# Optimization experiments

Measured on AMD Instinct MI355X. Metric: run time of the kernel, lower is better.

Reference implementation:

```python
import jax, jax.numpy as jnp
import numpy as np

B, S, N, D = 4, 4, 2048, 2048  # batch, residual streams, seq len, model dim


def rmsnorm(x, gamma, eps=1e-12):
    # F.normalize(x, dim=-1) * sqrt(d) * (gamma + 1)
    n = jnp.sqrt(jnp.sum(x * x, axis=-1, keepdims=True))
    return x / jnp.maximum(n, eps) * (x.shape[-1] ** 0.5) * (gamma + 1.0)


def setup_inputs() -> dict:
    key = jax.random.key(0)
    k0, k1, k2, k3 = jax.random.split(key, 4)
    residuals = jax.random.normal(k0, (B * S, N, D), dtype=jnp.float32)
    gamma = (jax.random.normal(k1, (D,), dtype=jnp.float32) * 0.02)
    # ProjActScale weights are zero-init in the module; use small random values
    # so the dynamic paths are numerically exercised.
    w_alpha = jax.random.normal(k2, (S + 1, D), dtype=jnp.float32) * 0.02
    w_beta = jax.random.normal(k3, (1, D), dtype=jnp.float32) * 0.02
    scale_alpha = jnp.asarray(0.01, dtype=jnp.float32)
    scale_beta = jnp.asarray(0.01, dtype=jnp.float32)
    # static_alpha = cat([init_alpha0, eye(S)], dim=1), layer_index=0 -> one-hot row 0
    init_alpha0 = np.zeros((S, 1), dtype=np.float32)
    init_alpha0[0, 0] = 1.0
    static_alpha = jnp.asarray(np.concatenate([init_alpha0, np.eye(S, dtype=np.float32)], axis=1))
    static_beta = jnp.ones((S,), dtype=jnp.float32)
    return dict(residuals=residuals, gamma=gamma, w_alpha=w_alpha, scale_alpha=scale_alpha,
                static_alpha=static_alpha, w_beta=w_beta, scale_beta=scale_beta,
                static_beta=static_beta)


def reference(residuals, gamma, w_alpha, scale_alpha, static_alpha, w_beta, scale_beta, static_beta):
    bs, n, d = residuals.shape
    s = static_beta.shape[0]
    b = bs // s
    # '(b s) n d -> b n s d'
    x = residuals.reshape(b, s, n, d).transpose(0, 2, 1, 3)
    normed = rmsnorm(x, gamma)
    # dynamic alpha / beta: zero-bias linear -> tanh -> scale
    dyn_alpha = jnp.tanh(jnp.einsum('bnsd,td->bnst', normed, w_alpha)) * scale_alpha
    alpha = dyn_alpha + static_alpha                      # (b, n, s, s+1)
    dyn_beta = jnp.tanh(jnp.einsum('bnsd,od->bnso', normed, w_beta))[..., 0] * scale_beta
    beta = dyn_beta + static_beta                         # (b, n, s)
    # width connection: mix residual streams
    mix = jnp.einsum('bnst,bnsd->bntd', alpha, x)         # (b, n, s+1, d)
    branch_input = mix[:, :, 0, :]                        # (b, n, d)
    res = mix[:, :, 1:, :]                                # (b, n, s, d)
    # identity branch (module has branch=None; the add_residual closure applies this)
    branch_out = branch_input
    # depth connection: outer product with beta, add residuals
    res = branch_out[:, :, None, :] * beta[..., None] + res
    # 'b n s d -> (b s) n d'
    out = res.transpose(0, 2, 1, 3).reshape(bs, n, d)
    return out
```

## Files before the change

### kernel.cpp

```cpp
#include <hip/hip_runtime.h>
#include <math.h>

#define NB 4
#define NS 4
#define NN 2048
#define ND 2048
#define NTHREADS 512
#define KPB 4
#define SQRT_D 45.254833995939045f

typedef float f32x4 __attribute__((ext_vector_type(4)));

#define GLOAD(dst, addr) \
    asm volatile("global_load_dwordx4 %0, %1, off" : "=&v"(dst) : "v"(addr) : "memory")

#define VM_WAIT_PREFETCH() do {                                \
    asm volatile("s_waitcnt vmcnt(4)" ::: "memory");           \
    __builtin_amdgcn_sched_barrier(0); } while (0)

#define SHIP(I, H, M_) {                                      \
    const float keep_ = hi_ ? v[(I)+(H)] : v[(I)];            \
    const float give_ = hi_ ? v[(I)] : v[(I)+(H)];            \
    v[(I)] = keep_ + __shfl_xor(give_, (M_)); }

#define BUTTERFLY()                                                          \
    { const bool hi_ = (lane & 1) != 0;                                      \
      SHIP(0,16,1)  SHIP(1,16,1)  SHIP(2,16,1)  SHIP(3,16,1)                 \
      SHIP(4,16,1)  SHIP(5,16,1)  SHIP(6,16,1)  SHIP(7,16,1)                 \
      SHIP(8,16,1)  SHIP(9,16,1)  SHIP(10,16,1) SHIP(11,16,1)                \
      SHIP(12,16,1) SHIP(13,16,1) SHIP(14,16,1) SHIP(15,16,1) }              \
    { const bool hi_ = (lane & 2) != 0;                                      \
      SHIP(0,8,2) SHIP(1,8,2) SHIP(2,8,2) SHIP(3,8,2)                        \
      SHIP(4,8,2) SHIP(5,8,2) SHIP(6,8,2) SHIP(7,8,2) }                      \
    { const bool hi_ = (lane & 4) != 0;                                      \
      SHIP(0,4,4) SHIP(1,4,4) SHIP(2,4,4) SHIP(3,4,4) }                      \
    { const bool hi_ = (lane & 8) != 0;                                      \
      SHIP(0,2,8) SHIP(1,2,8) }                                              \
    { const bool hi_ = (lane & 16) != 0;                                     \
      SHIP(0,1,16) }

#define ITER(XC0, XC1, XC2, XC3, XN0, XN1, XN2, XN3, K, PREF, WAIT)          \
  {                                                                          \
    if (WAIT) VM_WAIT_PREFETCH();                                            \
    float v[32];                                                             \
    _Pragma("unroll") for (int q = 0; q < 32; ++q) v[q] = 0.f;               \
    {                                                                        \
      f32x4 g4 = *(const f32x4*)(gamma + d);                                 \
      _Pragma("unroll") for (int e = 0; e < 4; ++e) {                        \
        v[0]  = __builtin_fmaf(XC0[e], XC0[e], v[0]);                        \
        v[7]  = __builtin_fmaf(XC1[e], XC1[e], v[7]);                        \
        v[14] = __builtin_fmaf(XC2[e], XC2[e], v[14]);                       \
        v[21] = __builtin_fmaf(XC3[e], XC3[e], v[21]);                       \
      }                                                                      \
      _Pragma("unroll") for (int j = 0; j < 6; ++j) {                        \
        const float* wsrc = (j < 5) ? (w_alpha + (size_t)j * ND + d)         \
                                    : (w_beta + d);                          \
        f32x4 w4 = *(const f32x4*)wsrc;                                      \
        f32x4 wg = w4 + w4 * g4;                        \
        _Pragma("unroll") for (int e = 0; e < 4; ++e) {                      \
          v[1 + j]  = __builtin_fmaf(XC0[e], wg[e], v[1 + j]);               \
          v[8 + j]  = __builtin_fmaf(XC1[e], wg[e], v[8 + j]);               \
          v[15 + j] = __builtin_fmaf(XC2[e], wg[e], v[15 + j]);              \
          v[22 + j] = __builtin_fmaf(XC3[e], wg[e], v[22 + j]);              \
        }                                                                    \
      }                                                                      \
    }                                                                        \
        \
    if (PREF) {                                                              \
      const float* np_ = xp + ((K) + 1) * ND;                                \
      GLOAD(XN0, np_);                                                       \
      GLOAD(XN1, np_ + row_stride);                                          \
      GLOAD(XN2, np_ + 2 * row_stride);                                      \
      GLOAD(XN3, np_ + 3 * row_stride);                                      \
    }                                                                        \
    BUTTERFLY()                                                              \
    const float tot##K = v[0] + __shfl_xor(v[0], 32);                        \
    if (lane < 32) red[wave][bidx] = tot##K;                                 \
    __syncthreads();                                                         \
    if (tid < 24) {                                                          \
      float ssq_ = 0.f, dot_ = 0.f;                                          \
      _Pragma("unroll") for (int w = 0; w < 8; ++w) {                        \
        ssq_ += red[w][es * 7];                                              \
        dot_ += red[w][es * 7 + 1 + ej];                                     \
      }                                                                      \
      const float rs_ = SQRT_D / fmaxf(sqrtf(ssq_), 1e-12f);                 \
      asb[es][ej] = __builtin_fmaf(tanhf(dot_ * rs_),                        \
                                   (ej < 5) ? sa : sb, stat);                \
    }                                                                        \
    __syncthreads();                                                         \
    {                                                                        \
      float M[NS][NS];                                                       \
      _Pragma("unroll") for (int so = 0; so < NS; ++so)                      \
        _Pragma("unroll") for (int si = 0; si < NS; ++si)                    \
          M[so][si] = __builtin_fmaf(asb[so][5], asb[si][0],                 \
                                     asb[si][so + 1]);                       \
      float* op_ = op + (K) * ND;                                            \
      _Pragma("unroll") for (int so = 0; so < NS; ++so) {                    \
        f32x4 o;                                                             \
        _Pragma("unroll") for (int e = 0; e < 4; ++e)                        \
          o[e] = M[so][0] * XC0[e] + M[so][1] * XC1[e]                       \
               + M[so][2] * XC2[e] + M[so][3] * XC3[e];                      \
        __builtin_nontemporal_store(o, (f32x4*)(op_ + (size_t)so * row_stride)); \
      }                                                                      \
    }                                                                        \
  }

__global__ __launch_bounds__(NTHREADS, 4)
void hyperconn_kernel(const float* __restrict__ residuals,
                      const float* __restrict__ gamma,
                      const float* __restrict__ w_alpha,
                      const float* __restrict__ scale_alpha,
                      const float* __restrict__ static_alpha,
                      const float* __restrict__ w_beta,
                      const float* __restrict__ scale_beta,
                      const float* __restrict__ static_beta,
                      float* __restrict__ out)
{
    __shared__ float red[8][32];
    __shared__ float asb[NS][6];

    const int tid  = threadIdx.x;
    const int blk  = blockIdx.x;
    const int b    = blk >> 9;
    const int n0   = (blk & 511) * KPB;
    const int wave = tid >> 6;
    const int lane = tid & 63;
    const int d    = tid << 2;

    const size_t row_stride = (size_t)NN * ND;
    const float* xp = residuals + (size_t)(b * NS) * row_stride + (size_t)n0 * ND + d;
    float*       op = out       + (size_t)(b * NS) * row_stride + (size_t)n0 * ND + d;

    const float sa = scale_alpha[0], sb = scale_beta[0];
    const int t24 = (tid < 24) ? tid : 0;
    const int es = t24 / 6, ej = t24 % 6;
    const float stat = (ej < 5) ? static_alpha[es * 5 + ej] : static_beta[es];
    const int bidx = ((lane & 1) << 4) | ((lane & 2) << 2) | (lane & 4)
                   | ((lane & 8) >> 2) | ((lane & 16) >> 4);

    f32x4 a0 = *(const f32x4*)(xp);
    f32x4 a1 = *(const f32x4*)(xp + row_stride);
    f32x4 a2 = *(const f32x4*)(xp + 2 * row_stride);
    f32x4 a3 = *(const f32x4*)(xp + 3 * row_stride);
    f32x4 c0, c1, c2, c3;

    ITER(a0, a1, a2, a3, c0, c1, c2, c3, 0, 1, 0)
    ITER(c0, c1, c2, c3, a0, a1, a2, a3, 1, 1, 1)
    ITER(a0, a1, a2, a3, c0, c1, c2, c3, 2, 1, 1)
    ITER(c0, c1, c2, c3, a0, a1, a2, a3, 3, 0, 1)
}

extern "C" void kernel_launch(void* const* d_in, const int* in_sizes, int n_in,
                              void* d_out, int out_size, void* d_ws, size_t ws_size,
                              hipStream_t stream) {
    const float* residuals    = (const float*)d_in[0];
    const float* gamma        = (const float*)d_in[1];
    const float* w_alpha      = (const float*)d_in[2];
    const float* scale_alpha  = (const float*)d_in[3];
    const float* static_alpha = (const float*)d_in[4];
    const float* w_beta       = (const float*)d_in[5];
    const float* scale_beta   = (const float*)d_in[6];
    const float* static_beta  = (const float*)d_in[7];
    float* out = (float*)d_out;

    const int grid = NB * NN / KPB;
    hyperconn_kernel<<<grid, NTHREADS, 0, stream>>>(
        residuals, gamma, w_alpha, scale_alpha, static_alpha,
        w_beta, scale_beta, static_beta, out);
}
```

Baseline: 84.69 us.

## Prefetch next residual row via async global-to-LDS double buffer

Replaces the register-based prefetch of the next sequence row with direct global_load_lds copies into a double-buffered shared-memory tile. Each wave copies its own slice, and each iteration reads its four streams back from LDS after a vmcnt wait. The prefetch is now issued after the reduction barriers, so it overlaps the mixing and output stores. This lowers register pressure, but the 64 KB LDS tile per block reduces how many blocks fit on a CU and adds LDS read traffic.

```diff
diff --git a/kernel.cpp b/kernel.cpp
--- a/kernel.cpp
+++ b/kernel.cpp
@@ -11,12 +11,15 @@
 
 typedef float f32x4 __attribute__((ext_vector_type(4)));
 
-#define GLOAD(dst, addr) \
-    asm volatile("global_load_dwordx4 %0, %1, off" : "=&v"(dst) : "v"(addr) : "memory")
+typedef __attribute__((address_space(3))) void lds_void_t;
+typedef const __attribute__((address_space(1))) void glb_void_t;
+#define ASYNC_COPY16(g, l) \
+    __builtin_amdgcn_global_load_lds((glb_void_t*)(g), (lds_void_t*)(l), 16, 0, 0)
 
-#define VM_WAIT_PREFETCH() do {                                \
-    asm volatile("s_waitcnt vmcnt(4)" ::: "memory");           \
+#define VMW_(N) do {                                           \
+    asm volatile("s_waitcnt vmcnt(" #N ")" ::: "memory");      \
     __builtin_amdgcn_sched_barrier(0); } while (0)
+#define VMW(N) VMW_(N)
 
 #define SHIP(I, H, M_) {                                      \
     const float keep_ = hi_ ? v[(I)+(H)] : v[(I)];            \
@@ -39,18 +42,22 @@
     { const bool hi_ = (lane & 16) != 0;                                     \
       SHIP(0,1,16) }
 
-#define ITER(XC0, XC1, XC2, XC3, XN0, XN1, XN2, XN3, K, PREF, WAIT)          \
+#define ITER(K, BF, PREF, WN)                                                \
   {                                                                          \
-    if (WAIT) VM_WAIT_PREFETCH();                                            \
+    VMW(WN);                                                                 \
+    f32x4 x0 = *(const f32x4*)&xbuf[BF][0][d];   \
+    f32x4 x1 = *(const f32x4*)&xbuf[BF][1][d];                               \
+    f32x4 x2 = *(const f32x4*)&xbuf[BF][2][d];                               \
+    f32x4 x3 = *(const f32x4*)&xbuf[BF][3][d];                               \
     float v[32];                                                             \
     _Pragma("unroll") for (int q = 0; q < 32; ++q) v[q] = 0.f;               \
     {                                                                        \
       f32x4 g4 = *(const f32x4*)(gamma + d);                                 \
       _Pragma("unroll") for (int e = 0; e < 4; ++e) {                        \
-        v[0]  = __builtin_fmaf(XC0[e], XC0[e], v[0]);                        \
-        v[7]  = __builtin_fmaf(XC1[e], XC1[e], v[7]);                        \
-        v[14] = __builtin_fmaf(XC2[e], XC2[e], v[14]);                       \
-        v[21] = __builtin_fmaf(XC3[e], XC3[e], v[21]);                       \
+        v[0]  = __builtin_fmaf(x0[e], x0[e], v[0]);                          \
+        v[7]  = __builtin_fmaf(x1[e], x1[e], v[7]);                          \
+        v[14] = __builtin_fmaf(x2[e], x2[e], v[14]);                         \
+        v[21] = __builtin_fmaf(x3[e], x3[e], v[21]);                         \
       }                                                                      \
       _Pragma("unroll") for (int j = 0; j < 6; ++j) {                        \
         const float* wsrc = (j < 5) ? (w_alpha + (size_t)j * ND + d)         \
@@ -58,20 +65,12 @@
         f32x4 w4 = *(const f32x4*)wsrc;                                      \
         f32x4 wg = w4 + w4 * g4;                        \
         _Pragma("unroll") for (int e = 0; e < 4; ++e) {                      \
-          v[1 + j]  = __builtin_fmaf(XC0[e], wg[e], v[1 + j]);               \
-          v[8 + j]  = __builtin_fmaf(XC1[e], wg[e], v[8 + j]);               \
-          v[15 + j] = __builtin_fmaf(XC2[e], wg[e], v[15 + j]);              \
-          v[22 + j] = __builtin_fmaf(XC3[e], wg[e], v[22 + j]);              \
+          v[1 + j]  = __builtin_fmaf(x0[e], wg[e], v[1 + j]);                \
+          v[8 + j]  = __builtin_fmaf(x1[e], wg[e], v[8 + j]);                \
+          v[15 + j] = __builtin_fmaf(x2[e], wg[e], v[15 + j]);               \
+          v[22 + j] = __builtin_fmaf(x3[e], wg[e], v[22 + j]);               \
         }                                                                    \
       }                                                                      \
-    }                                                                        \
-        \
-    if (PREF) {                                                              \
-      const float* np_ = xp + ((K) + 1) * ND;                                \
-      GLOAD(XN0, np_);                                                       \
-      GLOAD(XN1, np_ + row_stride);                                          \
-      GLOAD(XN2, np_ + 2 * row_stride);                                      \
-      GLOAD(XN3, np_ + 3 * row_stride);                                      \
     }                                                                        \
     BUTTERFLY()                                                              \
     const float tot##K = v[0] + __shfl_xor(v[0], 32);                        \
@@ -88,6 +87,16 @@
                                    (ej < 5) ? sa : sb, stat);                \
     }                                                                        \
     __syncthreads();                                                         \
+      \
+      \
+    if (PREF) {                                                              \
+      const float* np_ = xp + ((K) + 1) * ND;                                \
+      ASYNC_COPY16(np_,                  &xbuf[(BF) ^ 1][0][wave << 8]);     \
+      ASYNC_COPY16(np_ + row_stride,     &xbuf[(BF) ^ 1][1][wave << 8]);     \
+      ASYNC_COPY16(np_ + 2 * row_stride, &xbuf[(BF) ^ 1][2][wave << 8]);     \
+      ASYNC_COPY16(np_ + 3 * row_stride, &xbuf[(BF) ^ 1][3][wave << 8]);     \
+      __builtin_amdgcn_sched_barrier(0);         \
+    }                                                                        \
     {                                                                        \
       float M[NS][NS];                                                       \
       _Pragma("unroll") for (int so = 0; so < NS; ++so)                      \
@@ -98,8 +107,8 @@
       _Pragma("unroll") for (int so = 0; so < NS; ++so) {                    \
         f32x4 o;                                                             \
         _Pragma("unroll") for (int e = 0; e < 4; ++e)                        \
-          o[e] = M[so][0] * XC0[e] + M[so][1] * XC1[e]                       \
-               + M[so][2] * XC2[e] + M[so][3] * XC3[e];                      \
+          o[e] = M[so][0] * x0[e] + M[so][1] * x1[e]                         \
+               + M[so][2] * x2[e] + M[so][3] * x3[e];                        \
         __builtin_nontemporal_store(o, (f32x4*)(op_ + (size_t)so * row_stride)); \
       }                                                                      \
     }                                                                        \
@@ -116,6 +125,7 @@
                       const float* __restrict__ static_beta,
                       float* __restrict__ out)
 {
+    __shared__ float xbuf[2][NS][ND];
     __shared__ float red[8][32];
     __shared__ float asb[NS][6];
 
@@ -138,16 +148,15 @@
     const int bidx = ((lane & 1) << 4) | ((lane & 2) << 2) | (lane & 4)
                    | ((lane & 8) >> 2) | ((lane & 16) >> 4);
 
-    f32x4 a0 = *(const f32x4*)(xp);
-    f32x4 a1 = *(const f32x4*)(xp + row_stride);
-    f32x4 a2 = *(const f32x4*)(xp + 2 * row_stride);
-    f32x4 a3 = *(const f32x4*)(xp + 3 * row_stride);
-    f32x4 c0, c1, c2, c3;
+    ASYNC_COPY16(xp,                  &xbuf[0][0][wave << 8]);
+    ASYNC_COPY16(xp + row_stride,     &xbuf[0][1][wave << 8]);
+    ASYNC_COPY16(xp + 2 * row_stride, &xbuf[0][2][wave << 8]);
+    ASYNC_COPY16(xp + 3 * row_stride, &xbuf[0][3][wave << 8]);
 
-    ITER(a0, a1, a2, a3, c0, c1, c2, c3, 0, 1, 0)
-    ITER(c0, c1, c2, c3, a0, a1, a2, a3, 1, 1, 1)
-    ITER(a0, a1, a2, a3, c0, c1, c2, c3, 2, 1, 1)
-    ITER(c0, c1, c2, c3, a0, a1, a2, a3, 3, 0, 1)
+    ITER(0, 0, 1, 0)
+    ITER(1, 1, 1, 4)
+    ITER(2, 0, 1, 4)
+    ITER(3, 1, 0, 4)
 }
 
 extern "C" void kernel_launch(void* const* d_in, const int* in_sizes, int n_in,
```

Result: slower. 87.82 us (+3.7%).
